# Kernel optimization log

Hardware: AMD Instinct MI355X
Metric: run time of the kernel (lower is better)

The kernel has to match this reference:

```python
import jax, jax.numpy as jnp
import numpy as np

B, A, I, D = 4, 32, 512, 256


def setup_inputs() -> dict:
    key = jax.random.key(0)
    k0, k1, kw1, kw2, ka1, ka2 = jax.random.split(key, 6)
    return {
        "i0": jax.random.normal(k0, (B, A, I, D), dtype=jnp.float32),
        "i1": jax.random.normal(k1, (B, A, I, D), dtype=jnp.float32),
        "W1": jax.random.normal(kw1, (D, D), dtype=jnp.float32) * 0.02,
        "W2": jax.random.normal(kw2, (D, D), dtype=jnp.float32) * 0.02,
        "attn1": jax.random.normal(ka1, (D, D), dtype=jnp.float32) * 0.02,
        "attn2": jax.random.normal(ka2, (D, D), dtype=jnp.float32) * 0.02,
    }


def reference(i0, i1, W1, W2, attn1, attn2):
    # Bilinear gating scores: sum_j sum_k x1[...,j] * A[j,k] * x0[...,k] -> [b,a,i]
    g0 = jax.nn.sigmoid(jnp.einsum('baij,jk,baik->bai', i1, attn1, i0))
    g1 = jax.nn.sigmoid(jnp.einsum('baij,jk,baik->bai', i0, attn2, i1))
    # Gated residual: x += x * gate
    r0 = i0 + i0 * g0[..., None]
    r1 = i1 + i1 * g1[..., None]
    # Dual projection sum
    return jnp.einsum('baij,jk->baik', r0, W1) + jnp.einsum('baij,jk->baik', r1, W2)
```

## Files before the change

kernel.cpp:

```cpp
#include <hip/hip_runtime.h>

#define D256 256
#define TOTROWS 65536
#define BM 32
#define LDW 264
#define NBLK (TOTROWS / BM)
#define NT 512

typedef unsigned short u16;
typedef unsigned int u32;
typedef __attribute__((ext_vector_type(8))) short bf16x8;
typedef __attribute__((ext_vector_type(16))) float f32x16;

__device__ __forceinline__ float b2f(u16 u) {
  union { u32 i; float f; } v; v.i = ((u32)u) << 16; return v.f;
}
__device__ __forceinline__ u16 f2b(float f) {
  union { float f; u32 i; } v; v.f = f;
  return (u16)((v.i + 0x7fffu + ((v.i >> 16) & 1u)) >> 16);
}

__global__ void build_wfrag(const float* __restrict__ a1,
                            const float* __restrict__ a2,
                            const float* __restrict__ W1,
                            const float* __restrict__ W2,
                            u16* __restrict__ Wf) {
  const int m = blockIdx.y;
  const int idx = blockIdx.x * 256 + threadIdx.x;
  int col, c;
  const float* src;
  if (m < 2) {
    col = idx >> 5; c = idx & 31; src = m ? a2 : a1;
  } else {
    col = idx & 255; c = idx >> 8; src = (m == 3) ? W2 : W1;
  }
  const int kk0 = c * 8;
  const int p = col >> 5, l31 = col & 31, k = c >> 1, lh = c & 1;
  const int ln = lh * 32 + l31;
  u16* dst = Wf + m * 65536 + ((p * 16 + k) * 64 + ln) * 8;
  u16 v[8];
  if (m < 2) {
#pragma unroll
    for (int j = 0; j < 8; j++) v[j] = f2b(src[col * 256 + kk0 + j]);
  } else {
#pragma unroll
    for (int j = 0; j < 8; j++) v[j] = f2b(src[(kk0 + j) * 256 + col]);
  }
  ushort4 lo, hi;
  lo.x = v[0]; lo.y = v[1]; lo.z = v[2]; lo.w = v[3];
  hi.x = v[4]; hi.y = v[5]; hi.z = v[6]; hi.w = v[7];
  ((ushort4*)dst)[0] = lo;
  ((ushort4*)dst)[1] = hi;
}

__device__ __forceinline__ void reduce_accum(float v[16], float* sp,
                                             int l31, int lh) {
#pragma unroll
  for (int r = 0; r < 8; r++) {
    float a = v[r]     + __shfl_xor(v[r],     1, 32);
    float b = v[r + 8] + __shfl_xor(v[r + 8], 1, 32);
    v[r] = (l31 & 1) ? b : a;
  }
#pragma unroll
  for (int r = 0; r < 4; r++) {
    float a = v[r]     + __shfl_xor(v[r],     2, 32);
    float b = v[r + 4] + __shfl_xor(v[r + 4], 2, 32);
    v[r] = (l31 & 2) ? b : a;
  }
#pragma unroll
  for (int r = 0; r < 2; r++) {
    float a = v[r]     + __shfl_xor(v[r],     4, 32);
    float b = v[r + 2] + __shfl_xor(v[r + 2], 4, 32);
    v[r] = (l31 & 4) ? b : a;
  }
  {
    float a = v[0] + __shfl_xor(v[0], 8, 32);
    float b = v[1] + __shfl_xor(v[1], 8, 32);
    v[0] = (l31 & 8) ? b : a;
  }
  v[0] += __shfl_xor(v[0], 16, 32);
  if (l31 < 16) {
    const int i = ((l31 & 1) << 3) | ((l31 & 2) << 1) | ((l31 & 4) >> 1) |
                  ((l31 & 8) >> 3);
    const int row = (i & 3) + 8 * (i >> 2) + 4 * lh;
    atomicAdd(&sp[row], v[0]);
  }
}

__global__ __launch_bounds__(NT, 4)
void fused(const float* __restrict__ X0g, const float* __restrict__ X1g,
           const u16* __restrict__ Wf, float* __restrict__ outg) {
  __shared__ u16 lX0[BM][LDW];
  __shared__ u16 lX1[BM][LDW];
  __shared__ float sp0[BM], sp1[BM], sc0[BM], sc1[BM];

  const int t = threadIdx.x;
  const int row0 = blockIdx.x * BM;

  if (t < BM) { sp0[t] = 0.f; sp1[t] = 0.f; }

  {
    const float4* g0 = (const float4*)(X0g + (size_t)row0 * D256);
    const float4* g1 = (const float4*)(X1g + (size_t)row0 * D256);
    ushort4* s0 = (ushort4*)&lX0[0][0];
    ushort4* s1 = (ushort4*)&lX1[0][0];
#pragma unroll
    for (int i = 0; i < 4; i++) {
      const int e = i * NT + t;
      const int row = e >> 6;
      const int col = e & 63;
      float4 a = g0[e];
      float4 b = g1[e];
      ushort4 pa, pb;
      pa.x = f2b(a.x); pa.y = f2b(a.y); pa.z = f2b(a.z); pa.w = f2b(a.w);
      pb.x = f2b(b.x); pb.y = f2b(b.y); pb.z = f2b(b.z); pb.w = f2b(b.w);
      s0[row * 66 + col] = pa;
      s1[row * 66 + col] = pb;
    }
  }
  __syncthreads();

  const int ln  = t & 63;
  const int wv  = t >> 6;
  const int l31 = ln & 31;
  const int lh  = ln >> 5;
  const int cb  = wv * 32;

  const u16* wA1 = Wf + 0 * 65536 + (wv * 16) * 512 + ln * 8;
  const u16* wA2 = Wf + 1 * 65536 + (wv * 16) * 512 + ln * 8;
  const u16* wW1 = Wf + 2 * 65536 + (wv * 16) * 512 + ln * 8;
  const u16* wW2 = Wf + 3 * 65536 + (wv * 16) * 512 + ln * 8;

  {
    f32x16 G0, G1;
#pragma unroll
    for (int i = 0; i < 16; i++) { G0[i] = 0.f; G1[i] = 0.f; }

#pragma unroll 4
    for (int k = 0; k < 16; k++) {
      bf16x8 af0 = *(const bf16x8*)(&lX0[l31][k * 16 + lh * 8]);
      bf16x8 af1 = *(const bf16x8*)(&lX1[l31][k * 16 + lh * 8]);
      G0 = __builtin_amdgcn_mfma_f32_32x32x16_bf16(
          af0, *(const bf16x8*)(wA1 + k * 512), G0, 0, 0, 0);
      G1 = __builtin_amdgcn_mfma_f32_32x32x16_bf16(
          af1, *(const bf16x8*)(wA2 + k * 512), G1, 0, 0, 0);
    }

    float v[16];
#pragma unroll
    for (int r = 0; r < 16; r++) {
      const int row = (r & 3) + 8 * (r >> 2) + 4 * lh;
      v[r] = G0[r] * b2f(lX1[row][cb + l31]);
    }
    reduce_accum(v, sp0, l31, lh);
#pragma unroll
    for (int r = 0; r < 16; r++) {
      const int row = (r & 3) + 8 * (r >> 2) + 4 * lh;
      v[r] = G1[r] * b2f(lX0[row][cb + l31]);
    }
    reduce_accum(v, sp1, l31, lh);
  }
  __syncthreads();

  if (t < BM) {
    sc0[t] = 1.f + 1.f / (1.f + __expf(-sp0[t]));
  } else if (t < 2 * BM) {
    sc1[t - BM] = 1.f + 1.f / (1.f + __expf(-sp1[t - BM]));
  }
  __syncthreads();

  {
    f32x16 P0, P1;
#pragma unroll
    for (int i = 0; i < 16; i++) { P0[i] = 0.f; P1[i] = 0.f; }

#pragma unroll 4
    for (int k = 0; k < 16; k++) {
      bf16x8 af0 = *(const bf16x8*)(&lX0[l31][k * 16 + lh * 8]);
      bf16x8 af1 = *(const bf16x8*)(&lX1[l31][k * 16 + lh * 8]);
      P0 = __builtin_amdgcn_mfma_f32_32x32x16_bf16(
          af0, *(const bf16x8*)(wW1 + k * 512), P0, 0, 0, 0);
      P1 = __builtin_amdgcn_mfma_f32_32x32x16_bf16(
          af1, *(const bf16x8*)(wW2 + k * 512), P1, 0, 0, 0);
    }

    float* opb = outg + (size_t)row0 * 256 + cb;
#pragma unroll
    for (int q = 0; q < 4; q++) {
      float s0a[4], s1a[4];
      *(float4*)s0a = *(const float4*)&sc0[8 * q + 4 * lh];
      *(float4*)s1a = *(const float4*)&sc1[8 * q + 4 * lh];
#pragma unroll
      for (int j = 0; j < 4; j++) {
        const int r = q * 4 + j;
        const int row = j + 8 * q + 4 * lh;
        __builtin_nontemporal_store(s0a[j] * P0[r] + s1a[j] * P1[r],
                                    &opb[row * 256 + l31]);
      }
    }
  }
}

extern "C" void kernel_launch(void* const* d_in, const int* in_sizes, int n_in,
                              void* d_out, int out_size, void* d_ws, size_t ws_size,
                              hipStream_t stream) {
  const float* i0 = (const float*)d_in[0];
  const float* i1 = (const float*)d_in[1];
  const float* W1 = (const float*)d_in[2];
  const float* W2 = (const float*)d_in[3];
  const float* a1 = (const float*)d_in[4];
  const float* a2 = (const float*)d_in[5];
  u16* Wf = (u16*)d_ws;

  build_wfrag<<<dim3(32, 4), 256, 0, stream>>>(a1, a2, W1, W2, Wf);
  fused<<<NBLK, NT, 0, stream>>>(i0, i1, Wf, (float*)d_out);
}
```

Before: 207.3 us.

## Double row tile to 64 per block, reuse weight fragments, packed bf16 convert

Raises rows per block from 32 to 64, so each wave loads a weight fragment once and feeds two MFMAs, one per 32-row half. This halves global weight fragment traffic per row and halves the block count. The fp32-to-bf16 conversion now uses the packed v_cvt_pk_bf16_f32 instruction. The barrier before the projection GEMM moves to after it, so the gate sigmoid overlaps with the projection MFMAs. In exchange, LDS use doubles to about 67KB per block and register pressure rises with four accumulators, which may lower occupancy under launch_bounds(512,4).

```diff
diff --git a/kernel.cpp b/kernel.cpp
--- a/kernel.cpp
+++ b/kernel.cpp
@@ -2,7 +2,7 @@
 
 #define D256 256
 #define TOTROWS 65536
-#define BM 32
+#define BM 64
 #define LDW 264
 #define NBLK (TOTROWS / BM)
 #define NT 512
@@ -18,6 +18,11 @@
 __device__ __forceinline__ u16 f2b(float f) {
   union { float f; u32 i; } v; v.f = f;
   return (u16)((v.i + 0x7fffu + ((v.i >> 16) & 1u)) >> 16);
+}
+__device__ __forceinline__ u32 f2b2(float lo, float hi) {
+  u32 r;
+  asm("v_cvt_pk_bf16_f32 %0, %1, %2" : "=v"(r) : "v"(lo), "v"(hi));
+  return r;
 }
 
 __global__ void build_wfrag(const float* __restrict__ a1,
@@ -97,23 +102,24 @@
   const int t = threadIdx.x;
   const int row0 = blockIdx.x * BM;
 
-  if (t < BM) { sp0[t] = 0.f; sp1[t] = 0.f; }
+  if (t < BM) { sp0[t] = 0.f; }
+  else if (t < 2 * BM) { sp1[t - BM] = 0.f; }
 
   {
     const float4* g0 = (const float4*)(X0g + (size_t)row0 * D256);
     const float4* g1 = (const float4*)(X1g + (size_t)row0 * D256);
-    ushort4* s0 = (ushort4*)&lX0[0][0];
-    ushort4* s1 = (ushort4*)&lX1[0][0];
-#pragma unroll
-    for (int i = 0; i < 4; i++) {
+    uint2* s0 = (uint2*)&lX0[0][0];
+    uint2* s1 = (uint2*)&lX1[0][0];
+#pragma unroll 4
+    for (int i = 0; i < 8; i++) {
       const int e = i * NT + t;
       const int row = e >> 6;
       const int col = e & 63;
       float4 a = g0[e];
       float4 b = g1[e];
-      ushort4 pa, pb;
-      pa.x = f2b(a.x); pa.y = f2b(a.y); pa.z = f2b(a.z); pa.w = f2b(a.w);
-      pb.x = f2b(b.x); pb.y = f2b(b.y); pb.z = f2b(b.z); pb.w = f2b(b.w);
+      uint2 pa, pb;
+      pa.x = f2b2(a.x, a.y); pa.y = f2b2(a.z, a.w);
+      pb.x = f2b2(b.x, b.y); pb.y = f2b2(b.z, b.w);
       s0[row * 66 + col] = pa;
       s1[row * 66 + col] = pb;
     }
@@ -132,33 +138,50 @@
   const u16* wW2 = Wf + 3 * 65536 + (wv * 16) * 512 + ln * 8;
 
   {
-    f32x16 G0, G1;
-#pragma unroll
-    for (int i = 0; i < 16; i++) { G0[i] = 0.f; G1[i] = 0.f; }
-
-#pragma unroll 4
+    f32x16 G0a, G0b, G1a, G1b;
+#pragma unroll
+    for (int i = 0; i < 16; i++) { G0a[i] = 0.f; G0b[i] = 0.f;
+                                   G1a[i] = 0.f; G1b[i] = 0.f; }
+
+#pragma unroll 2
     for (int k = 0; k < 16; k++) {
-      bf16x8 af0 = *(const bf16x8*)(&lX0[l31][k * 16 + lh * 8]);
-      bf16x8 af1 = *(const bf16x8*)(&lX1[l31][k * 16 + lh * 8]);
-      G0 = __builtin_amdgcn_mfma_f32_32x32x16_bf16(
-          af0, *(const bf16x8*)(wA1 + k * 512), G0, 0, 0, 0);
-      G1 = __builtin_amdgcn_mfma_f32_32x32x16_bf16(
-          af1, *(const bf16x8*)(wA2 + k * 512), G1, 0, 0, 0);
+      bf16x8 w1 = *(const bf16x8*)(wA1 + k * 512);
+      bf16x8 w2 = *(const bf16x8*)(wA2 + k * 512);
+      bf16x8 a0a = *(const bf16x8*)(&lX0[l31][k * 16 + lh * 8]);
+      bf16x8 a0b = *(const bf16x8*)(&lX0[32 + l31][k * 16 + lh * 8]);
+      bf16x8 a1a = *(const bf16x8*)(&lX1[l31][k * 16 + lh * 8]);
+      bf16x8 a1b = *(const bf16x8*)(&lX1[32 + l31][k * 16 + lh * 8]);
+      G0a = __builtin_amdgcn_mfma_f32_32x32x16_bf16(a0a, w1, G0a, 0, 0, 0);
+      G0b = __builtin_amdgcn_mfma_f32_32x32x16_bf16(a0b, w1, G0b, 0, 0, 0);
+      G1a = __builtin_amdgcn_mfma_f32_32x32x16_bf16(a1a, w2, G1a, 0, 0, 0);
+      G1b = __builtin_amdgcn_mfma_f32_32x32x16_bf16(a1b, w2, G1b, 0, 0, 0);
     }
 
     float v[16];
 #pragma unroll
     for (int r = 0; r < 16; r++) {
       const int row = (r & 3) + 8 * (r >> 2) + 4 * lh;
-      v[r] = G0[r] * b2f(lX1[row][cb + l31]);
+      v[r] = G0a[r] * b2f(lX1[row][cb + l31]);
     }
     reduce_accum(v, sp0, l31, lh);
 #pragma unroll
     for (int r = 0; r < 16; r++) {
       const int row = (r & 3) + 8 * (r >> 2) + 4 * lh;
-      v[r] = G1[r] * b2f(lX0[row][cb + l31]);
+      v[r] = G0b[r] * b2f(lX1[32 + row][cb + l31]);
+    }
+    reduce_accum(v, sp0 + 32, l31, lh);
+#pragma unroll
+    for (int r = 0; r < 16; r++) {
+      const int row = (r & 3) + 8 * (r >> 2) + 4 * lh;
+      v[r] = G1a[r] * b2f(lX0[row][cb + l31]);
     }
     reduce_accum(v, sp1, l31, lh);
+#pragma unroll
+    for (int r = 0; r < 16; r++) {
+      const int row = (r & 3) + 8 * (r >> 2) + 4 * lh;
+      v[r] = G1b[r] * b2f(lX0[32 + row][cb + l31]);
+    }
+    reduce_accum(v, sp1 + 32, l31, lh);
   }
   __syncthreads();
 
@@ -167,35 +190,45 @@
   } else if (t < 2 * BM) {
     sc1[t - BM] = 1.f + 1.f / (1.f + __expf(-sp1[t - BM]));
   }
-  __syncthreads();
-
-  {
-    f32x16 P0, P1;
-#pragma unroll
-    for (int i = 0; i < 16; i++) { P0[i] = 0.f; P1[i] = 0.f; }
-
-#pragma unroll 4
+
+  {
+    f32x16 P0a, P0b, P1a, P1b;
+#pragma unroll
+    for (int i = 0; i < 16; i++) { P0a[i] = 0.f; P0b[i] = 0.f;
+                                   P1a[i] = 0.f; P1b[i] = 0.f; }
+
+#pragma unroll 2
     for (int k = 0; k < 16; k++) {
-      bf16x8 af0 = *(const bf16x8*)(&lX0[l31][k * 16 + lh * 8]);
-      bf16x8 af1 = *(const bf16x8*)(&lX1[l31][k * 16 + lh * 8]);
-      P0 = __builtin_amdgcn_mfma_f32_32x32x16_bf16(
-          af0, *(const bf16x8*)(wW1 + k * 512), P0, 0, 0, 0);
-      P1 = __builtin_amdgcn_mfma_f32_32x32x16_bf16(
-          af1, *(const bf16x8*)(wW2 + k * 512), P1, 0, 0, 0);
-    }
+      bf16x8 w1 = *(const bf16x8*)(wW1 + k * 512);
+      bf16x8 w2 = *(const bf16x8*)(wW2 + k * 512);
+      bf16x8 a0a = *(const bf16x8*)(&lX0[l31][k * 16 + lh * 8]);
+      bf16x8 a0b = *(const bf16x8*)(&lX0[32 + l31][k * 16 + lh * 8]);
+      bf16x8 a1a = *(const bf16x8*)(&lX1[l31][k * 16 + lh * 8]);
+      bf16x8 a1b = *(const bf16x8*)(&lX1[32 + l31][k * 16 + lh * 8]);
+      P0a = __builtin_amdgcn_mfma_f32_32x32x16_bf16(a0a, w1, P0a, 0, 0, 0);
+      P0b = __builtin_amdgcn_mfma_f32_32x32x16_bf16(a0b, w1, P0b, 0, 0, 0);
+      P1a = __builtin_amdgcn_mfma_f32_32x32x16_bf16(a1a, w2, P1a, 0, 0, 0);
+      P1b = __builtin_amdgcn_mfma_f32_32x32x16_bf16(a1b, w2, P1b, 0, 0, 0);
+    }
+
+    __syncthreads();
 
     float* opb = outg + (size_t)row0 * 256 + cb;
 #pragma unroll
     for (int q = 0; q < 4; q++) {
-      float s0a[4], s1a[4];
+      float s0a[4], s1a[4], s0b[4], s1b[4];
       *(float4*)s0a = *(const float4*)&sc0[8 * q + 4 * lh];
       *(float4*)s1a = *(const float4*)&sc1[8 * q + 4 * lh];
+      *(float4*)s0b = *(const float4*)&sc0[32 + 8 * q + 4 * lh];
+      *(float4*)s1b = *(const float4*)&sc1[32 + 8 * q + 4 * lh];
 #pragma unroll
       for (int j = 0; j < 4; j++) {
         const int r = q * 4 + j;
         const int row = j + 8 * q + 4 * lh;
-        __builtin_nontemporal_store(s0a[j] * P0[r] + s1a[j] * P1[r],
+        __builtin_nontemporal_store(s0a[j] * P0a[r] + s1a[j] * P1a[r],
                                     &opb[row * 256 + l31]);
+        __builtin_nontemporal_store(s0b[j] * P0b[r] + s1b[j] * P1b[r],
+                                    &opb[(32 + row) * 256 + l31]);
       }
     }
   }
```

Result: no change. 208.6 us (+0.7%).

## Process four row tiles per block with register-prefetched double-buffered LDS

Applied to the files above, without the earlier changes.

Each block now handles four 32-row tiles in sequence. The next tile's global loads are issued into registers before the current tile's MFMA work and written to a second LDS buffer afterward, so memory latency overlaps compute. Float-to-bf16 conversion now uses the packed v_cvt_pk_bf16_f32 instruction. The trade-offs are higher register and LDS use (launch bounds lowered to 2 blocks/CU), fewer blocks in the grid, and an extra barrier per tile.

```diff
diff --git a/kernel.cpp b/kernel.cpp
--- a/kernel.cpp
+++ b/kernel.cpp
@@ -4,7 +4,8 @@
 #define TOTROWS 65536
 #define BM 32
 #define LDW 264
-#define NBLK (TOTROWS / BM)
+#define TPB 4
+#define NBLKS (TOTROWS / (BM * TPB))
 #define NT 512
 
 typedef unsigned short u16;
@@ -18,6 +19,11 @@
 __device__ __forceinline__ u16 f2b(float f) {
   union { float f; u32 i; } v; v.f = f;
   return (u16)((v.i + 0x7fffu + ((v.i >> 16) & 1u)) >> 16);
+}
+__device__ __forceinline__ u32 f2b2(float lo, float hi) {
+  u32 r;
+  asm("v_cvt_pk_bf16_f32 %0, %1, %2" : "=v"(r) : "v"(lo), "v"(hi));
+  return r;
 }
 
 __global__ void build_wfrag(const float* __restrict__ a1,
@@ -29,14 +35,11 @@
   const int idx = blockIdx.x * 256 + threadIdx.x;
   int col, c;
   const float* src;
-  if (m < 2) {
-    col = idx >> 5; c = idx & 31; src = m ? a2 : a1;
-  } else {
-    col = idx & 255; c = idx >> 8; src = (m == 3) ? W2 : W1;
-  }
+  if (m < 2) { col = idx >> 5; c = idx & 31; src = m ? a2 : a1; }
+  else       { col = idx & 255; c = idx >> 8; src = (m == 3) ? W2 : W1; }
   const int kk0 = c * 8;
-  const int p = col >> 5, l31 = col & 31, k = c >> 1, lh = c & 1;
-  const int ln = lh * 32 + l31;
+  const int p = col >> 5, l31 = col & 31, lhh = c & 1, k = c >> 1;
+  const int ln = lhh * 32 + l31;
   u16* dst = Wf + m * 65536 + ((p * 16 + k) * 64 + ln) * 8;
   u16 v[8];
   if (m < 2) {
@@ -87,117 +90,141 @@
   }
 }
 
-__global__ __launch_bounds__(NT, 4)
+__global__ __launch_bounds__(NT, 2)
 void fused(const float* __restrict__ X0g, const float* __restrict__ X1g,
            const u16* __restrict__ Wf, float* __restrict__ outg) {
-  __shared__ u16 lX0[BM][LDW];
-  __shared__ u16 lX1[BM][LDW];
+  __shared__ u16 lX0[2][BM][LDW];
+  __shared__ u16 lX1[2][BM][LDW];
   __shared__ float sp0[BM], sp1[BM], sc0[BM], sc1[BM];
 
-  const int t = threadIdx.x;
-  const int row0 = blockIdx.x * BM;
-
-  if (t < BM) { sp0[t] = 0.f; sp1[t] = 0.f; }
-
-  {
-    const float4* g0 = (const float4*)(X0g + (size_t)row0 * D256);
-    const float4* g1 = (const float4*)(X1g + (size_t)row0 * D256);
-    ushort4* s0 = (ushort4*)&lX0[0][0];
-    ushort4* s1 = (ushort4*)&lX1[0][0];
-#pragma unroll
-    for (int i = 0; i < 4; i++) {
-      const int e = i * NT + t;
-      const int row = e >> 6;
-      const int col = e & 63;
-      float4 a = g0[e];
-      float4 b = g1[e];
-      ushort4 pa, pb;
-      pa.x = f2b(a.x); pa.y = f2b(a.y); pa.z = f2b(a.z); pa.w = f2b(a.w);
-      pb.x = f2b(b.x); pb.y = f2b(b.y); pb.z = f2b(b.z); pb.w = f2b(b.w);
-      s0[row * 66 + col] = pa;
-      s1[row * 66 + col] = pb;
-    }
-  }
-  __syncthreads();
-
+  const int t   = threadIdx.x;
   const int ln  = t & 63;
   const int wv  = t >> 6;
   const int l31 = ln & 31;
   const int lh  = ln >> 5;
   const int cb  = wv * 32;
 
+  const size_t base = (size_t)blockIdx.x * (TPB * BM);
+
   const u16* wA1 = Wf + 0 * 65536 + (wv * 16) * 512 + ln * 8;
   const u16* wA2 = Wf + 1 * 65536 + (wv * 16) * 512 + ln * 8;
   const u16* wW1 = Wf + 2 * 65536 + (wv * 16) * 512 + ln * 8;
   const u16* wW2 = Wf + 3 * 65536 + (wv * 16) * 512 + ln * 8;
 
+  auto stage_load = [&](size_t rowbase, float4* na, float4* nb) {
+    const float4* g0 = (const float4*)(X0g + rowbase * D256);
+    const float4* g1 = (const float4*)(X1g + rowbase * D256);
+#pragma unroll
+    for (int i = 0; i < 4; i++) {
+      na[i] = g0[i * NT + t];
+      nb[i] = g1[i * NT + t];
+    }
+  };
+  auto stage_write = [&](int b, const float4* na, const float4* nb) {
+    uint2* s0 = (uint2*)&lX0[b][0][0];
+    uint2* s1 = (uint2*)&lX1[b][0][0];
+#pragma unroll
+    for (int i = 0; i < 4; i++) {
+      const int e = i * NT + t;
+      const int row = e >> 6;
+      const int col = e & 63;
+      uint2 pa, pb;
+      pa.x = f2b2(na[i].x, na[i].y); pa.y = f2b2(na[i].z, na[i].w);
+      pb.x = f2b2(nb[i].x, nb[i].y); pb.y = f2b2(nb[i].z, nb[i].w);
+      s0[row * 66 + col] = pa;
+      s1[row * 66 + col] = pb;
+    }
+  };
+
+  if (t < BM) sp0[t] = 0.f;
+  else if (t < 2 * BM) sp1[t - BM] = 0.f;
+
   {
-    f32x16 G0, G1;
-#pragma unroll
-    for (int i = 0; i < 16; i++) { G0[i] = 0.f; G1[i] = 0.f; }
+    float4 pa[4], pb[4];
+    stage_load(base, pa, pb);
+    stage_write(0, pa, pb);
+  }
+  __syncthreads();
+
+  int buf = 0;
+  for (int tt = 0; tt < TPB; tt++) {
+    const size_t trow = base + (size_t)tt * BM;
+    const bool pf = (tt + 1 < TPB);
+
+    float4 na[4], nb[4];
+    if (pf) stage_load(trow + BM, na, nb);
+
+    {
+      f32x16 G0, G1;
+#pragma unroll
+      for (int i = 0; i < 16; i++) { G0[i] = 0.f; G1[i] = 0.f; }
 
 #pragma unroll 4
-    for (int k = 0; k < 16; k++) {
-      bf16x8 af0 = *(const bf16x8*)(&lX0[l31][k * 16 + lh * 8]);
-      bf16x8 af1 = *(const bf16x8*)(&lX1[l31][k * 16 + lh * 8]);
-      G0 = __builtin_amdgcn_mfma_f32_32x32x16_bf16(
-          af0, *(const bf16x8*)(wA1 + k * 512), G0, 0, 0, 0);
-      G1 = __builtin_amdgcn_mfma_f32_32x32x16_bf16(
-          af1, *(const bf16x8*)(wA2 + k * 512), G1, 0, 0, 0);
-    }
-
-    float v[16];
-#pragma unroll
-    for (int r = 0; r < 16; r++) {
-      const int row = (r & 3) + 8 * (r >> 2) + 4 * lh;
-      v[r] = G0[r] * b2f(lX1[row][cb + l31]);
-    }
-    reduce_accum(v, sp0, l31, lh);
-#pragma unroll
-    for (int r = 0; r < 16; r++) {
-      const int row = (r & 3) + 8 * (r >> 2) + 4 * lh;
-      v[r] = G1[r] * b2f(lX0[row][cb + l31]);
-    }
-    reduce_accum(v, sp1, l31, lh);
-  }
-  __syncthreads();
-
-  if (t < BM) {
-    sc0[t] = 1.f + 1.f / (1.f + __expf(-sp0[t]));
-  } else if (t < 2 * BM) {
-    sc1[t - BM] = 1.f + 1.f / (1.f + __expf(-sp1[t - BM]));
-  }
-  __syncthreads();
-
-  {
-    f32x16 P0, P1;
-#pragma unroll
-    for (int i = 0; i < 16; i++) { P0[i] = 0.f; P1[i] = 0.f; }
+      for (int k = 0; k < 16; k++) {
+        bf16x8 af0 = *(const bf16x8*)(&lX0[buf][l31][k * 16 + lh * 8]);
+        bf16x8 af1 = *(const bf16x8*)(&lX1[buf][l31][k * 16 + lh * 8]);
+        G0 = __builtin_amdgcn_mfma_f32_32x32x16_bf16(
+            af0, *(const bf16x8*)(wA1 + k * 512), G0, 0, 0, 0);
+        G1 = __builtin_amdgcn_mfma_f32_32x32x16_bf16(
+            af1, *(const bf16x8*)(wA2 + k * 512), G1, 0, 0, 0);
+      }
+
+      float v[16];
+#pragma unroll
+      for (int r = 0; r < 16; r++) {
+        const int row = (r & 3) + 8 * (r >> 2) + 4 * lh;
+        v[r] = G0[r] * b2f(lX1[buf][row][cb + l31]);
+      }
+      reduce_accum(v, sp0, l31, lh);
+#pragma unroll
+      for (int r = 0; r < 16; r++) {
+        const int row = (r & 3) + 8 * (r >> 2) + 4 * lh;
+        v[r] = G1[r] * b2f(lX0[buf][row][cb + l31]);
+      }
+      reduce_accum(v, sp1, l31, lh);
+    }
+    __syncthreads();
+
+    if (t < BM)          { sc0[t] = 1.f + 1.f / (1.f + __expf(-sp0[t]));
+                           sp0[t] = 0.f; }
+    else if (t < 2 * BM) { sc1[t - BM] = 1.f + 1.f / (1.f + __expf(-sp1[t - BM]));
+                           sp1[t - BM] = 0.f; }
+    __syncthreads();
+
+    {
+      f32x16 P0, P1;
+#pragma unroll
+      for (int i = 0; i < 16; i++) { P0[i] = 0.f; P1[i] = 0.f; }
 
 #pragma unroll 4
-    for (int k = 0; k < 16; k++) {
-      bf16x8 af0 = *(const bf16x8*)(&lX0[l31][k * 16 + lh * 8]);
-      bf16x8 af1 = *(const bf16x8*)(&lX1[l31][k * 16 + lh * 8]);
-      P0 = __builtin_amdgcn_mfma_f32_32x32x16_bf16(
-          af0, *(const bf16x8*)(wW1 + k * 512), P0, 0, 0, 0);
-      P1 = __builtin_amdgcn_mfma_f32_32x32x16_bf16(
-          af1, *(const bf16x8*)(wW2 + k * 512), P1, 0, 0, 0);
-    }
-
-    float* opb = outg + (size_t)row0 * 256 + cb;
-#pragma unroll
-    for (int q = 0; q < 4; q++) {
-      float s0a[4], s1a[4];
-      *(float4*)s0a = *(const float4*)&sc0[8 * q + 4 * lh];
-      *(float4*)s1a = *(const float4*)&sc1[8 * q + 4 * lh];
-#pragma unroll
-      for (int j = 0; j < 4; j++) {
-        const int r = q * 4 + j;
-        const int row = j + 8 * q + 4 * lh;
-        __builtin_nontemporal_store(s0a[j] * P0[r] + s1a[j] * P1[r],
-                                    &opb[row * 256 + l31]);
-      }
-    }
+      for (int k = 0; k < 16; k++) {
+        bf16x8 af0 = *(const bf16x8*)(&lX0[buf][l31][k * 16 + lh * 8]);
+        bf16x8 af1 = *(const bf16x8*)(&lX1[buf][l31][k * 16 + lh * 8]);
+        P0 = __builtin_amdgcn_mfma_f32_32x32x16_bf16(
+            af0, *(const bf16x8*)(wW1 + k * 512), P0, 0, 0, 0);
+        P1 = __builtin_amdgcn_mfma_f32_32x32x16_bf16(
+            af1, *(const bf16x8*)(wW2 + k * 512), P1, 0, 0, 0);
+      }
+
+      float* opb = outg + trow * D256 + cb;
+#pragma unroll
+      for (int q = 0; q < 4; q++) {
+        float s0a[4], s1a[4];
+        *(float4*)s0a = *(const float4*)&sc0[8 * q + 4 * lh];
+        *(float4*)s1a = *(const float4*)&sc1[8 * q + 4 * lh];
+#pragma unroll
+        for (int j = 0; j < 4; j++) {
+          const int r = q * 4 + j;
+          const int row = j + 8 * q + 4 * lh;
+          __builtin_nontemporal_store(s0a[j] * P0[r] + s1a[j] * P1[r],
+                                      &opb[row * D256 + l31]);
+        }
+      }
+    }
+
+    if (pf) stage_write(buf ^ 1, na, nb);
+    __syncthreads();
+    buf ^= 1;
   }
 }
 
@@ -213,5 +240,5 @@
   u16* Wf = (u16*)d_ws;
 
   build_wfrag<<<dim3(32, 4), 256, 0, stream>>>(a1, a2, W1, W2, Wf);
-  fused<<<NBLK, NT, 0, stream>>>(i0, i1, Wf, (float*)d_out);
-}
+  fused<<<NBLKS, NT, 0, stream>>>(i0, i1, Wf, (float*)d_out);
+}
```

Result: slower. 236.8 us (+14.2%).

## Merge gate and projection MFMA loops, use packed bf16 convert, drop sigmoid barrier

Applied to the files above, without the earlier changes.

Merges the gate-score MFMA loop and the output-projection MFMA loop into one K loop, so each bf16 A fragment is read from LDS once and feeds four accumulators. The per-row sigmoid scale is now computed by every thread at store time instead of in a separate phase, which removes one __syncthreads and the sc0/sc1 shared arrays. The fp32-to-bf16 staging conversion uses the packed v_cvt_pk_bf16_f32 instruction instead of manual rounding. In exchange, four f32x16 accumulators are live at once, raising VGPR/AGPR pressure under launch_bounds(512,4), and the sigmoid is computed redundantly across threads.

```diff
diff --git a/kernel.cpp b/kernel.cpp
--- a/kernel.cpp
+++ b/kernel.cpp
@@ -18,6 +18,11 @@
 __device__ __forceinline__ u16 f2b(float f) {
   union { float f; u32 i; } v; v.f = f;
   return (u16)((v.i + 0x7fffu + ((v.i >> 16) & 1u)) >> 16);
+}
+__device__ __forceinline__ u32 f2b2(float lo, float hi) {
+  u32 r;
+  asm("v_cvt_pk_bf16_f32 %0, %1, %2" : "=v"(r) : "v"(lo), "v"(hi));
+  return r;
 }
 
 __global__ void build_wfrag(const float* __restrict__ a1,
@@ -29,14 +34,11 @@
   const int idx = blockIdx.x * 256 + threadIdx.x;
   int col, c;
   const float* src;
-  if (m < 2) {
-    col = idx >> 5; c = idx & 31; src = m ? a2 : a1;
-  } else {
-    col = idx & 255; c = idx >> 8; src = (m == 3) ? W2 : W1;
-  }
+  if (m < 2) { col = idx >> 5; c = idx & 31; src = m ? a2 : a1; }
+  else       { col = idx & 255; c = idx >> 8; src = (m == 3) ? W2 : W1; }
   const int kk0 = c * 8;
-  const int p = col >> 5, l31 = col & 31, k = c >> 1, lh = c & 1;
-  const int ln = lh * 32 + l31;
+  const int p = col >> 5, l31 = col & 31, lhh = c & 1, k = c >> 1;
+  const int ln = lhh * 32 + l31;
   u16* dst = Wf + m * 65536 + ((p * 16 + k) * 64 + ln) * 8;
   u16 v[8];
   if (m < 2) {
@@ -92,18 +94,19 @@
            const u16* __restrict__ Wf, float* __restrict__ outg) {
   __shared__ u16 lX0[BM][LDW];
   __shared__ u16 lX1[BM][LDW];
-  __shared__ float sp0[BM], sp1[BM], sc0[BM], sc1[BM];
+  __shared__ float sp0[BM], sp1[BM];
 
   const int t = threadIdx.x;
   const int row0 = blockIdx.x * BM;
 
-  if (t < BM) { sp0[t] = 0.f; sp1[t] = 0.f; }
+  if (t < BM) sp0[t] = 0.f;
+  else if (t < 2 * BM) sp1[t - BM] = 0.f;
 
   {
     const float4* g0 = (const float4*)(X0g + (size_t)row0 * D256);
     const float4* g1 = (const float4*)(X1g + (size_t)row0 * D256);
-    ushort4* s0 = (ushort4*)&lX0[0][0];
-    ushort4* s1 = (ushort4*)&lX1[0][0];
+    uint2* s0 = (uint2*)&lX0[0][0];
+    uint2* s1 = (uint2*)&lX1[0][0];
 #pragma unroll
     for (int i = 0; i < 4; i++) {
       const int e = i * NT + t;
@@ -111,9 +114,9 @@
       const int col = e & 63;
       float4 a = g0[e];
       float4 b = g1[e];
-      ushort4 pa, pb;
-      pa.x = f2b(a.x); pa.y = f2b(a.y); pa.z = f2b(a.z); pa.w = f2b(a.w);
-      pb.x = f2b(b.x); pb.y = f2b(b.y); pb.z = f2b(b.z); pb.w = f2b(b.w);
+      uint2 pa, pb;
+      pa.x = f2b2(a.x, a.y); pa.y = f2b2(a.z, a.w);
+      pb.x = f2b2(b.x, b.y); pb.y = f2b2(b.z, b.w);
       s0[row * 66 + col] = pa;
       s1[row * 66 + col] = pb;
     }
@@ -131,21 +134,26 @@
   const u16* wW1 = Wf + 2 * 65536 + (wv * 16) * 512 + ln * 8;
   const u16* wW2 = Wf + 3 * 65536 + (wv * 16) * 512 + ln * 8;
 
-  {
-    f32x16 G0, G1;
-#pragma unroll
-    for (int i = 0; i < 16; i++) { G0[i] = 0.f; G1[i] = 0.f; }
+  f32x16 G0, G1, P0, P1;
+#pragma unroll
+  for (int i = 0; i < 16; i++) { G0[i] = 0.f; G1[i] = 0.f;
+                                 P0[i] = 0.f; P1[i] = 0.f; }
 
 #pragma unroll 4
-    for (int k = 0; k < 16; k++) {
-      bf16x8 af0 = *(const bf16x8*)(&lX0[l31][k * 16 + lh * 8]);
-      bf16x8 af1 = *(const bf16x8*)(&lX1[l31][k * 16 + lh * 8]);
-      G0 = __builtin_amdgcn_mfma_f32_32x32x16_bf16(
-          af0, *(const bf16x8*)(wA1 + k * 512), G0, 0, 0, 0);
-      G1 = __builtin_amdgcn_mfma_f32_32x32x16_bf16(
-          af1, *(const bf16x8*)(wA2 + k * 512), G1, 0, 0, 0);
-    }
-
+  for (int k = 0; k < 16; k++) {
+    bf16x8 af0 = *(const bf16x8*)(&lX0[l31][k * 16 + lh * 8]);
+    bf16x8 af1 = *(const bf16x8*)(&lX1[l31][k * 16 + lh * 8]);
+    bf16x8 wa1 = *(const bf16x8*)(wA1 + k * 512);
+    bf16x8 wa2 = *(const bf16x8*)(wA2 + k * 512);
+    bf16x8 ww1 = *(const bf16x8*)(wW1 + k * 512);
+    bf16x8 ww2 = *(const bf16x8*)(wW2 + k * 512);
+    G0 = __builtin_amdgcn_mfma_f32_32x32x16_bf16(af0, wa1, G0, 0, 0, 0);
+    P0 = __builtin_amdgcn_mfma_f32_32x32x16_bf16(af0, ww1, P0, 0, 0, 0);
+    G1 = __builtin_amdgcn_mfma_f32_32x32x16_bf16(af1, wa2, G1, 0, 0, 0);
+    P1 = __builtin_amdgcn_mfma_f32_32x32x16_bf16(af1, ww2, P1, 0, 0, 0);
+  }
+
+  {
     float v[16];
 #pragma unroll
     for (int r = 0; r < 16; r++) {
@@ -162,39 +170,17 @@
   }
   __syncthreads();
 
-  if (t < BM) {
-    sc0[t] = 1.f + 1.f / (1.f + __expf(-sp0[t]));
-  } else if (t < 2 * BM) {
-    sc1[t - BM] = 1.f + 1.f / (1.f + __expf(-sp1[t - BM]));
-  }
-  __syncthreads();
-
-  {
-    f32x16 P0, P1;
-#pragma unroll
-    for (int i = 0; i < 16; i++) { P0[i] = 0.f; P1[i] = 0.f; }
-
-#pragma unroll 4
-    for (int k = 0; k < 16; k++) {
-      bf16x8 af0 = *(const bf16x8*)(&lX0[l31][k * 16 + lh * 8]);
-      bf16x8 af1 = *(const bf16x8*)(&lX1[l31][k * 16 + lh * 8]);
-      P0 = __builtin_amdgcn_mfma_f32_32x32x16_bf16(
-          af0, *(const bf16x8*)(wW1 + k * 512), P0, 0, 0, 0);
-      P1 = __builtin_amdgcn_mfma_f32_32x32x16_bf16(
-          af1, *(const bf16x8*)(wW2 + k * 512), P1, 0, 0, 0);
-    }
-
+  {
     float* opb = outg + (size_t)row0 * 256 + cb;
 #pragma unroll
     for (int q = 0; q < 4; q++) {
-      float s0a[4], s1a[4];
-      *(float4*)s0a = *(const float4*)&sc0[8 * q + 4 * lh];
-      *(float4*)s1a = *(const float4*)&sc1[8 * q + 4 * lh];
 #pragma unroll
       for (int j = 0; j < 4; j++) {
         const int r = q * 4 + j;
         const int row = j + 8 * q + 4 * lh;
-        __builtin_nontemporal_store(s0a[j] * P0[r] + s1a[j] * P1[r],
+        const float s0 = 1.f + 1.f / (1.f + __expf(-sp0[row]));
+        const float s1 = 1.f + 1.f / (1.f + __expf(-sp1[row]));
+        __builtin_nontemporal_store(s0 * P0[r] + s1 * P1[r],
                                     &opb[row * 256 + l31]);
       }
     }
```

New measurement: 218.6 us. +5.5%, slower.
